# Kernel tuning notes

Measured on AMD Instinct MI355X. Metric: run time of the kernel, lower is better.

Reference implementation:

```python
import jax, jax.numpy as jnp
import numpy as np

N, C, T, V = 64, 64, 64, 25   # batch, channels, frames, joints
S, W = 8, 3                   # num_subset, window_size
IC = C // S                   # inter_channels = out_channels // num_subset = 8
OC = 64                       # out_channels
EPS = 1e-5


def setup_inputs() -> dict:
    key = jax.random.key(0)
    ks = jax.random.split(key, 24)
    std = 0.05
    x = jax.random.normal(ks[0], (N, C, V, T), jnp.float32)
    # fixed skeleton graphs (buffers, non-trainable)
    graph = (jax.random.uniform(ks[1], (S, V, V)) > 0.7).astype(jnp.float32)
    graph = jnp.clip(graph + jnp.eye(V, dtype=jnp.float32)[None], 0.0, 1.0)
    graph_a = jax.random.uniform(ks[2], (V, V), jnp.float32) / V
    # conv1x1 weights (out, in) + biases
    in_w = jax.random.normal(ks[3], (S * IC, C), jnp.float32) * std
    in_b = jax.random.normal(ks[4], (S * IC,), jnp.float32) * 0.01
    inup_w = jax.random.normal(ks[5], (S * IC, C), jnp.float32) * std
    inup_b = jax.random.normal(ks[6], (S * IC,), jnp.float32) * 0.01
    diff_w = jax.random.normal(ks[7], (C, C), jnp.float32) * std
    diff_b = jax.random.normal(ks[8], (C,), jnp.float32) * 0.01
    att0 = jnp.ones((1, S, W * V, V), jnp.float32) / V  # attention0s
    out_w = jax.random.normal(ks[9], (OC, S * C), jnp.float32) * std
    out_b = jax.random.normal(ks[10], (OC,), jnp.float32) * 0.01
    out_gamma = jnp.ones((OC,), jnp.float32)
    out_beta = jnp.zeros((OC,), jnp.float32)
    out_rm = jax.random.normal(ks[11], (OC,), jnp.float32) * 0.01
    out_rv = jnp.ones((OC,), jnp.float32)
    ff_w = jax.random.normal(ks[12], (OC, OC), jnp.float32) * std
    ff_b = jax.random.normal(ks[13], (OC,), jnp.float32) * 0.01
    ff_gamma = jnp.ones((OC,), jnp.float32)
    ff_beta = jnp.zeros((OC,), jnp.float32)
    ff_rm = jax.random.normal(ks[14], (OC,), jnp.float32) * 0.01
    ff_rv = jnp.ones((OC,), jnp.float32)
    return dict(x=x, graph=graph, graph_a=graph_a, in_w=in_w, in_b=in_b,
                inup_w=inup_w, inup_b=inup_b, diff_w=diff_w, diff_b=diff_b,
                att0=att0, out_w=out_w, out_b=out_b, out_gamma=out_gamma,
                out_beta=out_beta, out_rm=out_rm, out_rv=out_rv, ff_w=ff_w,
                ff_b=ff_b, ff_gamma=ff_gamma, ff_beta=ff_beta, ff_rm=ff_rm,
                ff_rv=ff_rv)


def _bn(x, g, b, m, v):  # inference-mode BatchNorm2d over channel dim 1
    scale = (g / jnp.sqrt(v + EPS))[None, :, None, None]
    return x * scale + (b - m * g / jnp.sqrt(v + EPS))[None, :, None, None]


def _leaky(x):
    return jnp.where(x > 0, x, 0.1 * x)


def _forward(x, graph, graph_a, in_w, in_b, inup_w, inup_b, diff_w, diff_b,
             att0, out_w, out_b, out_gamma, out_beta, out_rm, out_rv,
             ff_w, ff_b, ff_gamma, ff_beta, ff_rm, ff_rv):
    xp = jnp.transpose(x, (0, 1, 3, 2))          # (N,C,T,V)
    identity = xp
    # temporal window unfold: (N,C,T,W*V)
    xpad = jnp.pad(xp, ((0, 0), (0, 0), (1, 1), (0, 0)))
    upf = jnp.stack([xpad[:, :, w:w + T, :] for w in range(W)], axis=3)
    upf = upf.reshape(N, C, T, W * V)
    # q/k projections (conv1x1)
    k = (jnp.einsum('nctv,oc->notv', xp, in_w) + in_b[None, :, None, None])
    k = k.reshape(N, S, IC, T, V)
    q = (jnp.einsum('nctu,oc->notu', upf, inup_w) + inup_b[None, :, None, None])
    q = q.reshape(N, S, IC, T, W * V)
    att = jnp.einsum('nsctu,nsctv->nsuv', q, k) / (IC * T)  # (N,S,WV,V)
    # per-subset adjacency mask (graph[i] tiled over window rows)
    mask = jnp.tile(graph, (1, W, 1)) > 0                    # (S,WV,V)
    att = jnp.where(mask[None], att, jnp.float32(-9e15))
    att = jax.nn.softmax(att, axis=-1)
    # diff gate
    d = jnp.einsum('nctu,uv->nctv', xp, graph_a)
    d = jnp.einsum('nctv,oc->notv', d, diff_w) + diff_b[None, :, None, None]
    d = jnp.tile(d, (1, 1, 1, W)) - upf                      # (N,C,T,WV)
    d = d.reshape(N, S, C // S, T, W, V)
    gate = jax.nn.sigmoid(d.mean(axis=(2, 3, 5)))            # (N,S,W)
    att = att * jnp.tile(gate[..., None], (1, 1, V, 1))      # (N,S,WV,1) tiled
    att = att + att0
    # aggregate
    y = jnp.einsum('nctu,nsuv->nsctv', upf, att).reshape(N, S * C, T, V)
    y = _bn(jnp.einsum('nctv,oc->notv', y, out_w) + out_b[None, :, None, None],
            out_gamma, out_beta, out_rm, out_rv)
    y = _leaky(xp + y)                                       # downs1 = identity
    y = _bn(jnp.einsum('nctv,oc->notv', y, ff_w) + ff_b[None, :, None, None],
            ff_gamma, ff_beta, ff_rm, ff_rv)
    y = _leaky(xp + y)                                       # downs2 = identity
    z = jax.nn.relu(y + identity)
    return jnp.transpose(z, (0, 1, 3, 2))                    # back to (N,C,V,T)


def reference(x, graph, graph_a, in_w, in_b, inup_w, inup_b, diff_w, diff_b,
              att0, out_w, out_b, out_gamma, out_beta, out_rm, out_rv,
              ff_w, ff_b, ff_gamma, ff_beta, ff_rm, ff_rv):
    return _forward(x, graph, graph_a, in_w, in_b, inup_w, inup_b, diff_w,
                    diff_b, att0, out_w, out_b, out_gamma, out_beta, out_rm,
                    out_rv, ff_w, ff_b, ff_gamma, ff_beta, ff_rm, ff_rv)
```

## Files before the change

### kernel.cpp

```cpp
#include <hip/hip_runtime.h>
#include <hip/hip_bf16.h>
#include <math.h>

#define Nn 64
#define Cn 64
#define Tn 64
#define Vn 25
#define Sn 8
#define ICn 8
#define Wn 3
#define WVn 75

typedef __attribute__((ext_vector_type(8))) short s16x8;
typedef __attribute__((ext_vector_type(4))) short s16x4;
typedef __attribute__((ext_vector_type(4))) float f32x4;

#define MFMA16(a, b, c) __builtin_amdgcn_mfma_f32_16x16x32_bf16(a, b, c, 0, 0, 0)

static __device__ inline unsigned short f2bf(float f) {
    __hip_bfloat16 h = __float2bfloat16(f);
    return *reinterpret_cast<unsigned short*>(&h);
}
static __device__ inline float bf2f(unsigned short u) {
    union { unsigned int i; float f; } x;
    x.i = ((unsigned int)u) << 16;
    return x.f;
}

__global__ __launch_bounds__(64) void k_red(const float* __restrict__ x,
                                            const float* __restrict__ ga,
                                            const float* __restrict__ ow,
                                            const float* __restrict__ fw,
                                            float* __restrict__ red,
                                            unsigned short* __restrict__ owb,
                                            unsigned short* __restrict__ fwb) {
    const int c = blockIdx.x, n = blockIdx.y;
    const int lane = threadIdx.x;
    if (n == 0) {
        for (int j8 = 0; j8 < 8; ++j8) {
            const int q = c * 512 + j8 * 64 + lane;
            const int j = q & 7, ln = (q >> 3) & 63, fi = q >> 9;
            const int wvq = fi >> 4, ksq = fi & 15;
            owb[q] = f2bf(ow[(wvq * 16 + (ln & 15)) * 512 + ksq * 32 + (ln >> 4) * 8 + j]);
        }
        {
            const int q = c * 64 + lane;
            const int j = q & 7, ln = (q >> 3) & 63, fi = q >> 9;
            const int wvq = fi >> 1, ksq = fi & 1;
            fwb[q] = f2bf(fw[(wvq * 16 + (ln & 15)) * 64 + ksq * 32 + (ln >> 4) * 8 + j]);
        }
    }
    float rs = 0.f, r0 = 0.f, r63 = 0.f, xg = 0.f;
    if (lane < Vn) {
        const float* row = x + ((size_t)(n * Cn + c) * Vn + lane) * Tn;
        float g = 0.f;
        for (int j = 0; j < Vn; ++j) g += ga[lane * Vn + j];
        for (int t = 0; t < Tn; ++t) rs += row[t];
        r0 = row[0];
        r63 = row[Tn - 1];
        xg = rs * g;
    }
    for (int off = 32; off > 0; off >>= 1) {
        rs += __shfl_down(rs, off);
        r0 += __shfl_down(r0, off);
        r63 += __shfl_down(r63, off);
        xg += __shfl_down(xg, off);
    }
    if (lane == 0) {
        float* p = red + (size_t)(n * Cn + c) * 4;
        p[0] = rs; p[1] = r0; p[2] = r63; p[3] = xg;
    }
}

__global__ __launch_bounds__(256) void k_proj2(
    const float* __restrict__ x,
    const float* __restrict__ in_w, const float* __restrict__ in_b,
    const float* __restrict__ inup_w, const float* __restrict__ inup_b,
    unsigned short* __restrict__ pk, unsigned short* __restrict__ pq) {
    const int n = blockIdx.x, v = blockIdx.y;
    const int tid = threadIdx.x;
    const int lane = tid & 63, wv = tid >> 6;
    const int r16 = lane & 15, g4 = lane >> 4;

    __shared__ unsigned short WL[128 * 64];
    __shared__ unsigned short XT[64 * 64];
    __shared__ unsigned short CL[64 * 128];
    __shared__ float bias[128];

    if (tid < 128) bias[tid] = (tid < 64) ? in_b[tid] : inup_b[tid - 64];

    for (int idx = tid; idx < 2048; idx += 256) {
        const int o2 = idx >> 4, c4 = idx & 15;
        const float4 d = (o2 < 64)
            ? *(const float4*)(in_w + o2 * 64 + c4 * 4)
            : *(const float4*)(inup_w + (o2 - 64) * 64 + c4 * 4);
        s16x4 p;
        p[0] = (short)f2bf(d.x); p[1] = (short)f2bf(d.y);
        p[2] = (short)f2bf(d.z); p[3] = (short)f2bf(d.w);
        const int ch = c4 >> 1;
        *(s16x4*)&WL[o2 * 64 + (((ch ^ (o2 & 7))) << 3) + (c4 & 1) * 4] = p;
    }
    for (int idx = tid; idx < 1024; idx += 256) {
        const int c = idx >> 4, t4 = idx & 15;
        const float4 d = *(const float4*)(x +
            ((size_t)((n * Cn + c) * Vn + v)) * Tn + t4 * 4);
        const float dv[4] = {d.x, d.y, d.z, d.w};
#pragma unroll
        for (int jj = 0; jj < 4; ++jj) {
            const int t = t4 * 4 + jj;
            XT[t * 64 + (((c >> 3) ^ (t & 7)) << 3) + (c & 7)] = f2bf(dv[jj]);
        }
    }
    __syncthreads();

#pragma unroll
    for (int mi = 0; mi < 2; ++mi) {
        const int mt = wv * 2 + mi;
        const int o2r = mt * 16 + r16;
#pragma unroll
        for (int nt2 = 0; nt2 < 4; ++nt2) {
            const int t = nt2 * 16 + r16;
            f32x4 acc = (f32x4){0.f, 0.f, 0.f, 0.f};
#pragma unroll
            for (int ks = 0; ks < 2; ++ks) {
                const int ch = ks * 4 + g4;
                const s16x8 a = *(const s16x8*)&WL[o2r * 64 + ((ch ^ (o2r & 7)) << 3)];
                const s16x8 b = *(const s16x8*)&XT[t * 64 + ((ch ^ (t & 7)) << 3)];
                acc = MFMA16(a, b, acc);
            }
            const int tcol = nt2 * 16 + r16;
            const int ob = mt * 16 + g4 * 4;
            s16x4 p;
#pragma unroll
            for (int r = 0; r < 4; ++r) p[r] = f2bf(acc[r] + bias[ob + r]);
            const int ch = ob >> 3;
            *(s16x4*)&CL[tcol * 128 + ((ch ^ (tcol & 7)) << 3) + (ob & 7)] = p;
        }
    }
    __syncthreads();

    for (int jj = tid; jj < 1024; jj += 256) {
        const int t = jj & 63, p = jj >> 6;
        const s16x8 d = *(const s16x8*)&CL[t * 128 + ((p ^ (t & 7)) << 3)];
        const int s8 = p & 7;
        unsigned short* dst = (p < 8) ? pk : pq;
        *(s16x8*)(dst + ((((size_t)(n * Sn + s8) * Vn + v) * Tn + t) << 3)) = d;
    }
}

__global__ __launch_bounds__(256) void k_att3(
    const unsigned short* __restrict__ pq, const unsigned short* __restrict__ pk,
    const float* __restrict__ inup_b, const float* __restrict__ graph,
    const float* __restrict__ att0, const float* __restrict__ red,
    const float* __restrict__ diff_w, const float* __restrict__ diff_b,
    unsigned short* __restrict__ attB) {
    const int n = blockIdx.x, s = blockIdx.y;
    const int tid = threadIdx.x;
    const int lane = tid & 63, wv = tid >> 6;
    const int r16 = lane & 15, g4 = lane >> 4;

    __shared__ unsigned short QS[25 * 536];
    __shared__ unsigned short KS[32 * 512];
    __shared__ float attL[80 * 33];
    __shared__ float gp4[8][4];
    __shared__ float g3[3];

    if (tid < 8) {
        const int oc = s * ICn + tid;
        float a = 0.f;
        for (int c = 0; c < Cn; ++c)
            a += red[(n * Cn + c) * 4 + 3] * diff_w[oc * Cn + c];
        gp4[tid][0] = a + 1600.f * diff_b[oc];
        gp4[tid][1] = red[(n * Cn + oc) * 4 + 0];
        gp4[tid][2] = red[(n * Cn + oc) * 4 + 1];
        gp4[tid][3] = red[(n * Cn + oc) * 4 + 2];
    }
    for (int i = tid; i < 2048; i += 256) {
        const int t = i & 63, v = i >> 6;
        s16x8 d = (s16x8){0, 0, 0, 0, 0, 0, 0, 0};
        if (v < Vn)
            d = *(const s16x8*)(pk + ((((size_t)(n * Sn + s) * Vn + v) * Tn + t) << 3));
        *(s16x8*)&KS[v * 512 + ((t ^ (v & 7)) << 3)] = d;
    }
    for (int i = tid; i < 1600; i += 256) {
        const int t = i & 63, uu = i >> 6;
        const s16x8 d = *(const s16x8*)(pq +
            ((((size_t)(n * Sn + s) * Vn + uu) * Tn + t) << 3));
        *(s16x8*)&QS[uu * 536 + (t + 1) * 8] = d;
    }
    if (tid < 50) {
        const int uu = tid >> 1, slot = (tid & 1) * 65;
#pragma unroll
        for (int cc = 0; cc < ICn; ++cc)
            QS[uu * 536 + slot * 8 + cc] = f2bf(inup_b[s * ICn + cc]);
    }
    __syncthreads();

    for (int tile = wv; tile < 10; tile += 4) {
        const int mt = tile >> 1, nt = tile & 1;
        const int u = mt * 16 + r16;
        const int w = u / 25, uu = u % 25;
        const int v = nt * 16 + r16;
        const unsigned short* qbase = &QS[uu * 536 + (g4 + w) * 8];
        const unsigned short* kbase = &KS[v * 512];
        f32x4 acc = (f32x4){0.f, 0.f, 0.f, 0.f};
#pragma unroll
        for (int kb = 0; kb < 16; ++kb) {
            const s16x8 af = *(const s16x8*)(qbase + kb * 32);
            const s16x8 bf = *(const s16x8*)(kbase + (((kb * 4 + g4) ^ (v & 7)) << 3));
            acc = MFMA16(af, bf, acc);
        }
#pragma unroll
        for (int r = 0; r < 4; ++r)
            attL[(mt * 16 + g4 * 4 + r) * 33 + v] = acc[r];
    }
    if (tid == 0) {
        float sumd2 = 0.f, rsum = 0.f, rr0 = 0.f, rr63 = 0.f;
#pragma unroll
        for (int cc = 0; cc < 8; ++cc) {
            sumd2 += gp4[cc][0]; rsum += gp4[cc][1];
            rr0 += gp4[cc][2]; rr63 += gp4[cc][3];
        }
        const float inv = 1.f / 12800.f;
        g3[0] = 1.f / (1.f + expf(-(sumd2 - (rsum - rr63)) * inv));
        g3[1] = 1.f / (1.f + expf(-(sumd2 - rsum) * inv));
        g3[2] = 1.f / (1.f + expf(-(sumd2 - (rsum - rr0)) * inv));
    }
    __syncthreads();

    if (tid < WVn) {
        const int u = tid, u0 = u % Vn;
        const float* gr = graph + (s * Vn + u0) * Vn;
        float av[Vn];
        float mx = -1e30f;
#pragma unroll
        for (int v = 0; v < Vn; ++v) {
            float a = attL[u * 33 + v] * (1.f / 512.f);
            av[v] = (gr[v] > 0.f) ? a : -1e30f;
            mx = fmaxf(mx, av[v]);
        }
        float ssum = 0.f;
#pragma unroll
        for (int v = 0; v < Vn; ++v) {
            float e = (av[v] > -1e29f) ? expf(av[v] - mx) : 0.f;
            av[v] = e;
            ssum += e;
        }
        const float sc = g3[u % Wn] / ssum;
        const float* a0 = att0 + (s * WVn + u) * Vn;
#pragma unroll
        for (int v = 0; v < Vn; ++v) attL[u * 33 + v] = av[v] * sc + a0[v];
    }
    __syncthreads();

    unsigned short* ab = attB + ((size_t)(n * Sn + s)) * 3072;
    for (int idx = tid; idx < 3072; idx += 256) {
        const int j = idx & 7, ln = (idx >> 3) & 63, f = idx >> 9;
        const int k = f >> 1, nt = f & 1;
        const int v = nt * 16 + (ln & 15);
        const int vp = (ln >> 4) * 8 + j;
        float val = (v < Vn && vp < Vn) ? attL[(k * Vn + vp) * 33 + v] : 0.f;
        ab[idx] = f2bf(val);
    }
}

__global__ __launch_bounds__(256) void k_trans(const float* __restrict__ x,
                                               unsigned short* __restrict__ xT) {
    const int n = blockIdx.x, cb = blockIdx.y;
    const int c0 = cb * 4;
    const int tid = threadIdx.x;
    __shared__ unsigned short XL[4][25][66];

    for (int i = tid; i < 1600; i += 256) {
        const int piece = i & 15, row = i >> 4;
        const int cl = row / 25, v = row - cl * 25;
        const float4 d = *(const float4*)(x +
            ((size_t)((n * Cn + c0 + cl) * Vn + v)) * Tn + piece * 4);
        unsigned short* dst = &XL[cl][v][piece * 4];
        dst[0] = f2bf(d.x); dst[1] = f2bf(d.y); dst[2] = f2bf(d.z); dst[3] = f2bf(d.w);
    }
    __syncthreads();
    for (int j = tid; j < 1024; j += 256) {
        const int p = j & 3, cl = (j >> 2) & 3, t = j >> 4;
        const int v0 = (p ^ cl) * 8;
        unsigned short buf[8];
#pragma unroll
        for (int jj = 0; jj < 8; ++jj) {
            const int v = v0 + jj;
            buf[jj] = (v < Vn) ? XL[cl][v][t] : (unsigned short)0;
        }
        *(s16x8*)(xT + ((size_t)(n * Tn + t) * 2048) + (c0 + cl) * 32 + p * 8) =
            *(const s16x8*)buf;
    }
}

template <int STORE_T>
static __device__ void main_core(
    const unsigned short* __restrict__ xT, const unsigned short* __restrict__ attB,
    const unsigned short* __restrict__ out_wbf, const float* __restrict__ out_b,
    const float* __restrict__ og, const float* __restrict__ obeta,
    const float* __restrict__ orm, const float* __restrict__ orv,
    const unsigned short* __restrict__ ff_wbf, const float* __restrict__ ff_b,
    const float* __restrict__ fg, const float* __restrict__ fbeta,
    const float* __restrict__ frm, const float* __restrict__ frv,
    float* __restrict__ out, float* __restrict__ outT) {
    const int n = blockIdx.x, t = blockIdx.y;
    const int tid = threadIdx.x;
    const int lane = tid & 63, wv = tid >> 6;
    const int r16 = lane & 15, g4 = lane >> 4;

    __shared__ unsigned short xs3[3 * 2048];
    __shared__ unsigned short y2L[32 * 512];
    __shared__ unsigned short y1L[32 * 64];
    __shared__ float bnp[384];

    if (tid < 64) {
        int o = tid;
        float so = og[o] * rsqrtf(orv[o] + 1e-5f);
        bnp[o] = so; bnp[64 + o] = obeta[o] - orm[o] * so; bnp[128 + o] = out_b[o];
        float sf = fg[o] * rsqrtf(frv[o] + 1e-5f);
        bnp[192 + o] = sf; bnp[256 + o] = fbeta[o] - frm[o] * sf; bnp[320 + o] = ff_b[o];
    }
    for (int ch = tid; ch < 768; ch += 256) {
        const int kb = ch >> 8, off = ch & 255;
        const int tg = t - 1 + kb;
        s16x8 d = (s16x8){0, 0, 0, 0, 0, 0, 0, 0};
        if (tg >= 0 && tg < Tn)
            d = *(const s16x8*)(xT + ((size_t)(n * Tn + tg) * 2048) + off * 8);
        *(s16x8*)&xs3[ch * 8] = d;
    }
    __syncthreads();

    s16x8 af[4][3];
#pragma unroll
    for (int m = 0; m < 4; ++m) {
        const int c = m * 16 + r16;
#pragma unroll
        for (int kb = 0; kb < 3; ++kb)
            af[m][kb] = *(const s16x8*)&xs3[kb * 2048 + c * 32 + ((g4 ^ (c & 3)) << 3)];
    }
#pragma unroll
    for (int si = 0; si < 2; ++si) {
        const int s = wv * 2 + si;
        const unsigned short* aB = attB + ((size_t)(n * Sn + s)) * 3072;
        s16x8 bfr[3][2];
#pragma unroll
        for (int k = 0; k < 3; ++k)
#pragma unroll
            for (int nt = 0; nt < 2; ++nt)
                bfr[k][nt] = *(const s16x8*)(aB + (((k * 2 + nt) * 64 + lane) << 3));
#pragma unroll
        for (int m = 0; m < 4; ++m) {
            f32x4 c0 = (f32x4){0.f, 0.f, 0.f, 0.f};
            f32x4 c1 = (f32x4){0.f, 0.f, 0.f, 0.f};
#pragma unroll
            for (int kb = 0; kb < 3; ++kb) {
                c0 = MFMA16(af[m][kb], bfr[kb][0], c0);
                c1 = MFMA16(af[m][kb], bfr[kb][1], c1);
            }
            const int cw = m * 16 + g4 * 4;
            s16x4 p0, p1;
#pragma unroll
            for (int r = 0; r < 4; ++r) { p0[r] = f2bf(c0[r]); p1[r] = f2bf(c1[r]); }
            const int v0 = r16, v1 = 16 + r16;
            *(s16x4*)&y2L[v0 * 512 + (s * 8 + ((cw >> 3) ^ (v0 & 7))) * 8 + (cw & 7)] = p0;
            *(s16x4*)&y2L[v1 * 512 + (s * 8 + ((cw >> 3) ^ (v1 & 7))) * 8 + (cw & 7)] = p1;
        }
    }
    __syncthreads();

    f32x4 accO[2];
    accO[0] = (f32x4){0.f, 0.f, 0.f, 0.f};
    accO[1] = (f32x4){0.f, 0.f, 0.f, 0.f};
#pragma unroll
    for (int ks = 0; ks < 16; ++ks) {
        const s16x8 wa = *(const s16x8*)(out_wbf +
            ((((size_t)(wv * 16 + ks)) * 64 + lane) << 3));
        const int cidx = ks * 4 + g4;
        const int srow = cidx >> 3, lc = cidx & 7;
#pragma unroll
        for (int na = 0; na < 2; ++na) {
            const int v = na * 16 + r16;
            const s16x8 b = *(const s16x8*)&y2L[v * 512 + (srow * 8 + (lc ^ (v & 7))) * 8];
            accO[na] = MFMA16(wa, b, accO[na]);
        }
    }
    float xvc[2][4];
    const int ob = wv * 16 + g4 * 4;
#pragma unroll
    for (int na = 0; na < 2; ++na) {
        const int v = na * 16 + r16;
        s16x4 p;
#pragma unroll
        for (int r = 0; r < 4; ++r) {
            const int o = ob + r;
            const float xv = bf2f(xs3[2048 + o * 32 + ((((v >> 3)) ^ (o & 3)) << 3) + (v & 7)]);
            xvc[na][r] = xv;
            float val = (accO[na][r] + bnp[128 + o]) * bnp[o] + bnp[64 + o];
            float y1 = xv + val;
            y1 = (y1 > 0.f) ? y1 : 0.1f * y1;
            p[r] = f2bf(y1);
        }
        *(s16x4*)&y1L[v * 64 + (((ob >> 3) ^ (v & 7)) << 3) + (ob & 7)] = p;
    }
    __syncthreads();

    f32x4 accF[2];
    accF[0] = (f32x4){0.f, 0.f, 0.f, 0.f};
    accF[1] = (f32x4){0.f, 0.f, 0.f, 0.f};
#pragma unroll
    for (int ks = 0; ks < 2; ++ks) {
        const s16x8 fa = *(const s16x8*)(ff_wbf + (((wv * 2 + ks) * 64 + lane) << 3));
        const int cidx = ks * 4 + g4;
#pragma unroll
        for (int na = 0; na < 2; ++na) {
            const int v = na * 16 + r16;
            const s16x8 b = *(const s16x8*)&y1L[v * 64 + ((cidx ^ (v & 7)) << 3)];
            accF[na] = MFMA16(fa, b, accF[na]);
        }
    }
#pragma unroll
    for (int na = 0; na < 2; ++na) {
        const int v = na * 16 + r16;
        if (v < Vn) {
            float4 pv;
            float* pvp = (float*)&pv;
#pragma unroll
            for (int r = 0; r < 4; ++r) {
                const int o = ob + r;
                const float xv = xvc[na][r];
                float val = (accF[na][r] + bnp[320 + o]) * bnp[192 + o] + bnp[256 + o];
                float y2v = xv + val;
                y2v = (y2v > 0.f) ? y2v : 0.1f * y2v;
                float outv = y2v + xv;
                outv = (outv > 0.f) ? outv : 0.f;
                if (STORE_T) pvp[r] = outv;
                else out[((size_t)(n * Cn + o) * Vn + v) * Tn + t] = outv;
            }
            if (STORE_T)
                *(float4*)(outT + ((size_t)(n * Tn + t) * Vn + v) * 64 + ob) = pv;
        }
    }
}

__global__ __launch_bounds__(256, 3) void k_main11(
    const unsigned short* __restrict__ xT, const unsigned short* __restrict__ attB,
    const unsigned short* __restrict__ out_wbf, const float* __restrict__ out_b,
    const float* __restrict__ og, const float* __restrict__ obeta,
    const float* __restrict__ orm, const float* __restrict__ orv,
    const unsigned short* __restrict__ ff_wbf, const float* __restrict__ ff_b,
    const float* __restrict__ fg, const float* __restrict__ fbeta,
    const float* __restrict__ frm, const float* __restrict__ frv,
    float* __restrict__ out) {
    main_core<0>(xT, attB, out_wbf, out_b, og, obeta, orm, orv, ff_wbf, ff_b,
                 fg, fbeta, frm, frv, out, nullptr);
}

__global__ __launch_bounds__(256, 3) void k_main12(
    const unsigned short* __restrict__ xT, const unsigned short* __restrict__ attB,
    const unsigned short* __restrict__ out_wbf, const float* __restrict__ out_b,
    const float* __restrict__ og, const float* __restrict__ obeta,
    const float* __restrict__ orm, const float* __restrict__ orv,
    const unsigned short* __restrict__ ff_wbf, const float* __restrict__ ff_b,
    const float* __restrict__ fg, const float* __restrict__ fbeta,
    const float* __restrict__ frm, const float* __restrict__ frv,
    float* __restrict__ outT) {
    main_core<1>(xT, attB, out_wbf, out_b, og, obeta, orm, orv, ff_wbf, ff_b,
                 fg, fbeta, frm, frv, nullptr, outT);
}

__global__ __launch_bounds__(256) void k_out(const float* __restrict__ outT,
                                             float* __restrict__ out) {
    const int n = blockIdx.x, tc = blockIdx.y;
    const int t0 = tc * 4;
    const int tid = threadIdx.x;
    __shared__ float outL[4 * 1600];

#pragma unroll
    for (int tl = 0; tl < 4; ++tl) {
        const float* src = outT + ((size_t)(n * Tn + t0 + tl) * Vn) * 64;
        for (int i = tid; i < 1600; i += 256)
            outL[tl * 1600 + i] = src[i];
    }
    __syncthreads();
    for (int r = tid; r < 1600; r += 256) {
        const int v = r >> 6, o = r & 63;
        float4 pv;
        pv.x = outL[0 * 1600 + r];
        pv.y = outL[1 * 1600 + r];
        pv.z = outL[2 * 1600 + r];
        pv.w = outL[3 * 1600 + r];
        *(float4*)(out + ((size_t)(n * Cn + o) * Vn + v) * Tn + t0) = pv;
    }
}

extern "C" void kernel_launch(void* const* d_in, const int* in_sizes, int n_in,
                              void* d_out, int out_size, void* d_ws, size_t ws_size,
                              hipStream_t stream) {
    const float* x       = (const float*)d_in[0];
    const float* graph   = (const float*)d_in[1];
    const float* graph_a = (const float*)d_in[2];
    const float* in_w    = (const float*)d_in[3];
    const float* in_b    = (const float*)d_in[4];
    const float* inup_w  = (const float*)d_in[5];
    const float* inup_b  = (const float*)d_in[6];
    const float* diff_w  = (const float*)d_in[7];
    const float* diff_b  = (const float*)d_in[8];
    const float* att0    = (const float*)d_in[9];
    const float* out_w   = (const float*)d_in[10];
    const float* out_b   = (const float*)d_in[11];
    const float* og      = (const float*)d_in[12];
    const float* obeta   = (const float*)d_in[13];
    const float* orm     = (const float*)d_in[14];
    const float* orv     = (const float*)d_in[15];
    const float* ff_w    = (const float*)d_in[16];
    const float* ff_b    = (const float*)d_in[17];
    const float* fg      = (const float*)d_in[18];
    const float* fbeta   = (const float*)d_in[19];
    const float* frm     = (const float*)d_in[20];
    const float* frv     = (const float*)d_in[21];
    float* out = (float*)d_out;

    char* wsb = (char*)d_ws;
    float* red_ws  = (float*)(wsb);
    unsigned short* attB = (unsigned short*)(wsb + 71680);
    unsigned short* owb  = (unsigned short*)(wsb + 3217408);
    unsigned short* fwb  = (unsigned short*)(wsb + 3282944);
    unsigned short* pq = (unsigned short*)(wsb + 3291136);
    unsigned short* pk = (unsigned short*)(wsb + 16398336);
    unsigned short* xT = (unsigned short*)(wsb + 3291136);
    float* outT = (float*)(wsb + 20068352);
    const bool big = ws_size >= (size_t)46282752;

    k_red<<<dim3(Cn, Nn), 64, 0, stream>>>(x, graph_a, out_w, ff_w, red_ws, owb, fwb);
    k_proj2<<<dim3(Nn, Vn), 256, 0, stream>>>(x, in_w, in_b, inup_w, inup_b, pk, pq);
    k_att3<<<dim3(Nn, Sn), 256, 0, stream>>>(pq, pk, inup_b, graph, att0,
                                             red_ws, diff_w, diff_b, attB);
    k_trans<<<dim3(Nn, 16), 256, 0, stream>>>(x, xT);
    if (big) {
        k_main12<<<dim3(Nn, Tn), 256, 0, stream>>>(xT, attB, owb, out_b, og, obeta,
                                                   orm, orv, fwb, ff_b, fg, fbeta,
                                                   frm, frv, outT);
        k_out<<<dim3(Nn, Tn / 4), 256, 0, stream>>>(outT, out);
    } else {
        k_main11<<<dim3(Nn, Tn), 256, 0, stream>>>(xT, attB, owb, out_b, og, obeta,
                                                   orm, orv, fwb, ff_b, fg, fbeta,
                                                   frm, frv, out);
    }
}
```

Measured before the change: 104.6 us.

## Store transposed input in MFMA fragment order and load A operands directly

The transpose kernel now writes x in an MFMA-fragment-ready layout, so the main kernel loads its A fragments straight from global memory instead of staging three time slices through shared memory. Only the center time slice is kept in LDS, for the residual. That buffer is reused for the y1 intermediate after an extra barrier. Together these cut LDS use and allow launch bounds of 4 blocks per CU, trading LDS staging for more direct global loads and one more sync.

```diff
diff --git a/kernel.cpp b/kernel.cpp
--- a/kernel.cpp
+++ b/kernel.cpp
@@ -264,8 +264,8 @@
     }
 }
 
-__global__ __launch_bounds__(256) void k_trans(const float* __restrict__ x,
-                                               unsigned short* __restrict__ xT) {
+__global__ __launch_bounds__(256) void k_trans2(const float* __restrict__ x,
+                                                unsigned short* __restrict__ xTA) {
     const int n = blockIdx.x, cb = blockIdx.y;
     const int c0 = cb * 4;
     const int tid = threadIdx.x;
@@ -280,23 +280,24 @@
         dst[0] = f2bf(d.x); dst[1] = f2bf(d.y); dst[2] = f2bf(d.z); dst[3] = f2bf(d.w);
     }
     __syncthreads();
-    for (int j = tid; j < 1024; j += 256) {
-        const int p = j & 3, cl = (j >> 2) & 3, t = j >> 4;
-        const int v0 = (p ^ cl) * 8;
+    for (int j2 = tid; j2 < 1024; j2 += 256) {
+        const int g = j2 & 3, cl = (j2 >> 2) & 3, t = j2 >> 4;
+        const int c = c0 + cl;
         unsigned short buf[8];
 #pragma unroll
         for (int jj = 0; jj < 8; ++jj) {
-            const int v = v0 + jj;
+            const int v = g * 8 + jj;
             buf[jj] = (v < Vn) ? XL[cl][v][t] : (unsigned short)0;
         }
-        *(s16x8*)(xT + ((size_t)(n * Tn + t) * 2048) + (c0 + cl) * 32 + p * 8) =
+        const int m = c >> 4, l = (c & 15) + 16 * g;
+        *(s16x8*)(xTA + ((size_t)((n * Tn + t) * 4 + m)) * 512 + l * 8) =
             *(const s16x8*)buf;
     }
 }
 
 template <int STORE_T>
-static __device__ void main_core(
-    const unsigned short* __restrict__ xT, const unsigned short* __restrict__ attB,
+static __device__ void main14_core(
+    const unsigned short* __restrict__ xTA, const unsigned short* __restrict__ attB,
     const unsigned short* __restrict__ out_wbf, const float* __restrict__ out_b,
     const float* __restrict__ og, const float* __restrict__ obeta,
     const float* __restrict__ orm, const float* __restrict__ orv,
@@ -309,9 +310,8 @@
     const int lane = tid & 63, wv = tid >> 6;
     const int r16 = lane & 15, g4 = lane >> 4;
 
-    __shared__ unsigned short xs3[3 * 2048];
     __shared__ unsigned short y2L[32 * 512];
-    __shared__ unsigned short y1L[32 * 64];
+    __shared__ unsigned short ubuf[2048];
     __shared__ float bnp[384];
 
     if (tid < 64) {
@@ -321,24 +321,24 @@
         float sf = fg[o] * rsqrtf(frv[o] + 1e-5f);
         bnp[192 + o] = sf; bnp[256 + o] = fbeta[o] - frm[o] * sf; bnp[320 + o] = ff_b[o];
     }
-    for (int ch = tid; ch < 768; ch += 256) {
-        const int kb = ch >> 8, off = ch & 255;
+    {
+        const s16x8 d = *(const s16x8*)(xTA +
+            ((size_t)((n * Tn + t) * 4)) * 512 + tid * 8);
+        *(s16x8*)&ubuf[tid * 8] = d;
+    }
+    s16x8 af[4][3];
+#pragma unroll
+    for (int kb = 0; kb < 3; ++kb) {
         const int tg = t - 1 + kb;
-        s16x8 d = (s16x8){0, 0, 0, 0, 0, 0, 0, 0};
-        if (tg >= 0 && tg < Tn)
-            d = *(const s16x8*)(xT + ((size_t)(n * Tn + tg) * 2048) + off * 8);
-        *(s16x8*)&xs3[ch * 8] = d;
-    }
-    __syncthreads();
-
-    s16x8 af[4][3];
-#pragma unroll
-    for (int m = 0; m < 4; ++m) {
-        const int c = m * 16 + r16;
-#pragma unroll
-        for (int kb = 0; kb < 3; ++kb)
-            af[m][kb] = *(const s16x8*)&xs3[kb * 2048 + c * 32 + ((g4 ^ (c & 3)) << 3)];
-    }
+#pragma unroll
+        for (int m = 0; m < 4; ++m) {
+            af[m][kb] = (tg >= 0 && tg < Tn)
+                ? *(const s16x8*)(xTA + ((size_t)((n * Tn + tg) * 4 + m)) * 512 + lane * 8)
+                : (s16x8){0, 0, 0, 0, 0, 0, 0, 0};
+        }
+    }
+    __syncthreads();
+
 #pragma unroll
     for (int si = 0; si < 2; ++si) {
         const int s = wv * 2 + si;
@@ -385,23 +385,28 @@
             accO[na] = MFMA16(wa, b, accO[na]);
         }
     }
+    const int ob = wv * 16 + g4 * 4;
     float xvc[2][4];
-    const int ob = wv * 16 + g4 * 4;
+    s16x4 y1p[2];
 #pragma unroll
     for (int na = 0; na < 2; ++na) {
         const int v = na * 16 + r16;
-        s16x4 p;
 #pragma unroll
         for (int r = 0; r < 4; ++r) {
             const int o = ob + r;
-            const float xv = bf2f(xs3[2048 + o * 32 + ((((v >> 3)) ^ (o & 3)) << 3) + (v & 7)]);
+            const float xv = bf2f(ubuf[(o >> 4) * 512 + ((o & 15) + 16 * (v >> 3)) * 8 + (v & 7)]);
             xvc[na][r] = xv;
             float val = (accO[na][r] + bnp[128 + o]) * bnp[o] + bnp[64 + o];
             float y1 = xv + val;
             y1 = (y1 > 0.f) ? y1 : 0.1f * y1;
-            p[r] = f2bf(y1);
-        }
-        *(s16x4*)&y1L[v * 64 + (((ob >> 3) ^ (v & 7)) << 3) + (ob & 7)] = p;
+            y1p[na][r] = f2bf(y1);
+        }
+    }
+    __syncthreads();
+#pragma unroll
+    for (int na = 0; na < 2; ++na) {
+        const int v = na * 16 + r16;
+        *(s16x4*)&ubuf[v * 64 + (((ob >> 3) ^ (v & 7)) << 3) + (ob & 7)] = y1p[na];
     }
     __syncthreads();
 
@@ -415,7 +420,7 @@
 #pragma unroll
         for (int na = 0; na < 2; ++na) {
             const int v = na * 16 + r16;
-            const s16x8 b = *(const s16x8*)&y1L[v * 64 + ((cidx ^ (v & 7)) << 3)];
+            const s16x8 b = *(const s16x8*)&ubuf[v * 64 + ((cidx ^ (v & 7)) << 3)];
             accF[na] = MFMA16(fa, b, accF[na]);
         }
     }
@@ -443,8 +448,8 @@
     }
 }
 
-__global__ __launch_bounds__(256, 3) void k_main11(
-    const unsigned short* __restrict__ xT, const unsigned short* __restrict__ attB,
+__global__ __launch_bounds__(256, 4) void k_main14a(
+    const unsigned short* __restrict__ xTA, const unsigned short* __restrict__ attB,
     const unsigned short* __restrict__ out_wbf, const float* __restrict__ out_b,
     const float* __restrict__ og, const float* __restrict__ obeta,
     const float* __restrict__ orm, const float* __restrict__ orv,
@@ -452,12 +457,12 @@
     const float* __restrict__ fg, const float* __restrict__ fbeta,
     const float* __restrict__ frm, const float* __restrict__ frv,
     float* __restrict__ out) {
-    main_core<0>(xT, attB, out_wbf, out_b, og, obeta, orm, orv, ff_wbf, ff_b,
-                 fg, fbeta, frm, frv, out, nullptr);
-}
-
-__global__ __launch_bounds__(256, 3) void k_main12(
-    const unsigned short* __restrict__ xT, const unsigned short* __restrict__ attB,
+    main14_core<0>(xTA, attB, out_wbf, out_b, og, obeta, orm, orv, ff_wbf, ff_b,
+                   fg, fbeta, frm, frv, out, nullptr);
+}
+
+__global__ __launch_bounds__(256, 4) void k_main14b(
+    const unsigned short* __restrict__ xTA, const unsigned short* __restrict__ attB,
     const unsigned short* __restrict__ out_wbf, const float* __restrict__ out_b,
     const float* __restrict__ og, const float* __restrict__ obeta,
     const float* __restrict__ orm, const float* __restrict__ orv,
@@ -465,8 +470,8 @@
     const float* __restrict__ fg, const float* __restrict__ fbeta,
     const float* __restrict__ frm, const float* __restrict__ frv,
     float* __restrict__ outT) {
-    main_core<1>(xT, attB, out_wbf, out_b, og, obeta, orm, orv, ff_wbf, ff_b,
-                 fg, fbeta, frm, frv, nullptr, outT);
+    main14_core<1>(xTA, attB, out_wbf, out_b, og, obeta, orm, orv, ff_wbf, ff_b,
+                   fg, fbeta, frm, frv, nullptr, outT);
 }
 
 __global__ __launch_bounds__(256) void k_out(const float* __restrict__ outT,
@@ -528,7 +533,7 @@
     unsigned short* fwb  = (unsigned short*)(wsb + 3282944);
     unsigned short* pq = (unsigned short*)(wsb + 3291136);
     unsigned short* pk = (unsigned short*)(wsb + 16398336);
-    unsigned short* xT = (unsigned short*)(wsb + 3291136);
+    unsigned short* xTA = (unsigned short*)(wsb + 3291136);
     float* outT = (float*)(wsb + 20068352);
     const bool big = ws_size >= (size_t)46282752;
 
@@ -536,15 +541,15 @@
     k_proj2<<<dim3(Nn, Vn), 256, 0, stream>>>(x, in_w, in_b, inup_w, inup_b, pk, pq);
     k_att3<<<dim3(Nn, Sn), 256, 0, stream>>>(pq, pk, inup_b, graph, att0,
                                              red_ws, diff_w, diff_b, attB);
-    k_trans<<<dim3(Nn, 16), 256, 0, stream>>>(x, xT);
+    k_trans2<<<dim3(Nn, 16), 256, 0, stream>>>(x, xTA);
     if (big) {
-        k_main12<<<dim3(Nn, Tn), 256, 0, stream>>>(xT, attB, owb, out_b, og, obeta,
-                                                   orm, orv, fwb, ff_b, fg, fbeta,
-                                                   frm, frv, outT);
+        k_main14b<<<dim3(Nn, Tn), 256, 0, stream>>>(xTA, attB, owb, out_b, og, obeta,
+                                                    orm, orv, fwb, ff_b, fg, fbeta,
+                                                    frm, frv, outT);
         k_out<<<dim3(Nn, Tn / 4), 256, 0, stream>>>(outT, out);
     } else {
-        k_main11<<<dim3(Nn, Tn), 256, 0, stream>>>(xT, attB, owb, out_b, og, obeta,
-                                                   orm, orv, fwb, ff_b, fg, fbeta,
-                                                   frm, frv, out);
-    }
-}
+        k_main14a<<<dim3(Nn, Tn), 256, 0, stream>>>(xTA, attB, owb, out_b, og, obeta,
+                                                    orm, orv, fwb, ff_b, fg, fbeta,
+                                                    frm, frv, out);
+    }
+}
```

New measurement: 104.9 us. No clear change (+0.2%).
